# Kernel tuning notes

Measured on AMD Instinct MI355X. Metric: run time of the kernel, lower is better.

## Reference

```python
import jax, jax.numpy as jnp
import numpy as np


def positional_encoding(n_tokens, d_model, dtype=jnp.float32):
    # standard sinusoidal PE: pe[pos, 2i] = sin(pos / 10000^(2i/d)), pe[pos, 2i+1] = cos(...)
    pos = jnp.arange(n_tokens, dtype=dtype)[:, None]            # [n, 1]
    i = jnp.arange(0, d_model, 2, dtype=dtype)[None, :]         # [1, d/2]
    angle = pos / jnp.power(jnp.asarray(10000.0, dtype), i / d_model)
    pe = jnp.zeros((n_tokens, d_model), dtype)
    pe = pe.at[:, 0::2].set(jnp.sin(angle))
    pe = pe.at[:, 1::2].set(jnp.cos(angle))
    return pe


def layer_norm(x, gamma, beta, eps=1e-5):
    mu = jnp.mean(x, axis=-1, keepdims=True)
    var = jnp.var(x, axis=-1, keepdims=True)
    return (x - mu) * jax.lax.rsqrt(var + eps) * gamma + beta


def setup_inputs() -> dict:
    key = jax.random.key(0)
    ks = jax.random.split(key, 4)
    b, n, d = 4, 1024, 1024
    dh = 1024  # dim_hidden_linear
    s = 1.0 / np.sqrt(d)
    return {
        "token_embedding": jax.random.normal(ks[0], (b, n, d), jnp.float32),
        "ln_gamma": jnp.ones((d,), jnp.float32),
        "ln_beta": jnp.zeros((d,), jnp.float32),
        "Wq": jax.random.normal(ks[1], (d, dh), jnp.float32) * s,
        "bq": jnp.zeros((dh,), jnp.float32),
        "Wk": jax.random.normal(ks[2], (d, dh), jnp.float32) * s,
        "bk": jnp.zeros((dh,), jnp.float32),
        "Wv": jax.random.normal(ks[3], (d, dh), jnp.float32) * s,
        "bv": jnp.zeros((dh,), jnp.float32),
        "num_heads": 16,
    }


def reference(token_embedding, ln_gamma, ln_beta, Wq, bq, Wk, bk, Wv, bv, num_heads):
    b, n, d = token_embedding.shape
    pe = positional_encoding(n, d)                      # [n, d]
    x = token_embedding + pe[None, :, :]                # broadcast over batch
    x = layer_norm(x, ln_gamma, ln_beta)
    q = x @ Wq + bq                                     # [b, n, dh]
    k = x @ Wk + bk
    v = x @ Wv + bv
    dh = q.shape[-1]
    hd = dh // num_heads                                # per-head dim
    q = q.reshape(b, n, num_heads, hd)
    k = k.reshape(b, n, num_heads, hd)
    v = v.reshape(b, n, num_heads, hd)
    scale = 1.0 / jnp.sqrt(jnp.asarray(hd, q.dtype))
    scores = jnp.einsum("bqhd,bkhd->bhqk", q, k) * scale  # [b, h, n, n]
    attn = jax.nn.softmax(scores, axis=-1)
    out = jnp.einsum("bhqk,bkhd->bqhd", attn, v)          # [b, n, h, hd]
    return out.reshape(b, n, dh)
```

## Files before the change

kernel.cpp:

```cpp
#include <hip/hip_runtime.h>
#include <hip/hip_bf16.h>
#include <math.h>

typedef __attribute__((ext_vector_type(8))) short bf16x8;
typedef __attribute__((ext_vector_type(4))) short bf16x4;
typedef __attribute__((ext_vector_type(4))) float f32x4;

static __device__ __forceinline__ void gld16(const void* g, void* l) {
    __builtin_amdgcn_global_load_lds(
        (const __attribute__((address_space(1))) unsigned int*)g,
        (__attribute__((address_space(3))) unsigned int*)l, 16, 0, 0);
}

static __device__ __forceinline__ short f2bf_s(float f) {
    __hip_bfloat16 h = __float2bfloat16(f);
    short s;
    __builtin_memcpy(&s, &h, 2);
    return s;
}

__global__ __launch_bounds__(256) void peln_kernel(
    const float* __restrict__ emb,
    const float* __restrict__ gamma,
    const float* __restrict__ beta,
    __hip_bfloat16* __restrict__ x)
{
    const int row = blockIdx.x;
    const int t   = row & 1023;
    const int tid = threadIdx.x;

    float4 e = ((const float4*)(emb + (size_t)row * 1024))[tid];
    float v[4] = {e.x, e.y, e.z, e.w};
    float s = 0.f, ss = 0.f;
    #pragma unroll
    for (int kk = 0; kk < 4; ++kk) {
        int c = tid * 4 + kk;
        float ang = (float)t * exp2f(-13.287712379549449f * (float)(c >> 1) * (1.0f / 512.0f));
        float pe  = (c & 1) ? __cosf(ang) : __sinf(ang);
        v[kk] += pe;
        s  += v[kk];
        ss += v[kk] * v[kk];
    }
    #pragma unroll
    for (int off = 1; off < 64; off <<= 1) {
        s  += __shfl_xor(s, off);
        ss += __shfl_xor(ss, off);
    }
    __shared__ float red_s[4], red_ss[4];
    int wave = tid >> 6, lane = tid & 63;
    if (lane == 0) { red_s[wave] = s; red_ss[wave] = ss; }
    __syncthreads();
    float S  = red_s[0] + red_s[1] + red_s[2] + red_s[3];
    float SS = red_ss[0] + red_ss[1] + red_ss[2] + red_ss[3];
    float mu   = S * (1.0f / 1024.0f);
    float var  = SS * (1.0f / 1024.0f) - mu * mu;
    float rstd = rsqrtf(var + 1e-5f);
    #pragma unroll
    for (int kk = 0; kk < 4; ++kk) {
        int c = tid * 4 + kk;
        float y = (v[kk] - mu) * rstd * gamma[c] + beta[c];
        x[(size_t)row * 1024 + c] = __float2bfloat16(y);
    }
}

__global__ void wt_kernel(const float* __restrict__ Wq,
                          const float* __restrict__ Wk,
                          const float* __restrict__ Wv,
                          __hip_bfloat16* __restrict__ Wt)
{
    __shared__ __hip_bfloat16 tile[32][33];
    int zz = blockIdx.z;
    const float* src = (zz == 0) ? Wq : (zz == 1) ? Wk : Wv;
    __hip_bfloat16* dst = Wt + (size_t)zz * 1024 * 1024;
    int x0 = blockIdx.x * 32, y0 = blockIdx.y * 32;
    int tx = threadIdx.x, ty = threadIdx.y;
    #pragma unroll
    for (int kk = 0; kk < 4; ++kk)
        tile[ty + 8 * kk][tx] =
            __float2bfloat16(src[(size_t)(y0 + ty + 8 * kk) * 1024 + x0 + tx]);
    __syncthreads();
    #pragma unroll
    for (int kk = 0; kk < 4; ++kk)
        dst[(size_t)(x0 + ty + 8 * kk) * 1024 + y0 + tx] = tile[tx][ty + 8 * kk];
}

__global__ __launch_bounds__(256) void qkv_gemm(
    const __hip_bfloat16* __restrict__ X,
    const __hip_bfloat16* __restrict__ Wt,
    const float* __restrict__ bq,
    const float* __restrict__ bk,
    const float* __restrict__ bv,
    __hip_bfloat16* __restrict__ qkv)
{
    union SMem {
        struct { __hip_bfloat16 A[128 * 64]; __hip_bfloat16 B[128 * 64]; } s;
        __hip_bfloat16 C[128 * 132];
    };
    __shared__ __align__(16) SMem sm;

    const int id   = blockIdx.x;
    const int xcd  = id & 7;
    const int rest = id >> 3;
    const int j    = rest % 3;
    const int mblk = rest / 3;
    const int m0   = mblk * 128;
    const int n0   = (xcd * 3 + j) * 128;
    const int t    = n0 >> 10;
    const int nn0  = n0 & 1023;
    const __hip_bfloat16* W = Wt + (size_t)t * 1024 * 1024;

    const int tid  = threadIdx.x;
    const int wave = tid >> 6, lane = tid & 63;
    const int wm = wave & 1, wn = wave >> 1;
    const int lm = lane & 15, quad = lane >> 4;

    const int srow = lane >> 3;
    const int skc  = ((lane & 7) ^ srow) * 8;
    const int rbase = wave * 32;
    const __hip_bfloat16* gA = X + (size_t)(m0 + rbase + srow) * 1024 + skc;
    const __hip_bfloat16* gB = W + (size_t)(nn0 + rbase + srow) * 1024 + skc;
    __hip_bfloat16* lA = sm.s.A + rbase * 64;
    __hip_bfloat16* lB = sm.s.B + rbase * 64;

    f32x4 acc[4][4];
    #pragma unroll
    for (int i = 0; i < 4; ++i)
        #pragma unroll
        for (int jj = 0; jj < 4; ++jj)
            acc[i][jj] = (f32x4){0.f, 0.f, 0.f, 0.f};

    for (int k0 = 0; k0 < 1024; k0 += 64) {
        #pragma unroll
        for (int n = 0; n < 4; ++n) {
            gld16(gA + (size_t)n * 8 * 1024 + k0, lA + n * 8 * 64);
            gld16(gB + (size_t)n * 8 * 1024 + k0, lB + n * 8 * 64);
        }
        __syncthreads();

        bf16x8 a[2][4], b[2][4];
        #pragma unroll
        for (int ks = 0; ks < 2; ++ks) {
            #pragma unroll
            for (int i = 0; i < 4; ++i) {
                int row = wm * 64 + i * 16 + lm;
                a[ks][i] = *(const bf16x8*)(sm.s.A + (size_t)row * 64
                                            + (((ks * 4 + quad) ^ (lm & 7)) * 8));
            }
            #pragma unroll
            for (int jj = 0; jj < 4; ++jj) {
                int row = wn * 64 + jj * 16 + lm;
                b[ks][jj] = *(const bf16x8*)(sm.s.B + (size_t)row * 64
                                             + (((ks * 4 + quad) ^ (lm & 7)) * 8));
            }
        }
        __syncthreads();

        #pragma unroll
        for (int ks = 0; ks < 2; ++ks)
            #pragma unroll
            for (int i = 0; i < 4; ++i)
                #pragma unroll
                for (int jj = 0; jj < 4; ++jj)
                    acc[i][jj] = __builtin_amdgcn_mfma_f32_16x16x32_bf16(a[ks][i], b[ks][jj], acc[i][jj], 0, 0, 0);
    }

    const float* bias = (t == 0) ? bq : (t == 1) ? bk : bv;
    #pragma unroll
    for (int jj = 0; jj < 4; ++jj) {
        int col = wn * 64 + jj * 16 + lm;
        float bb = bias[nn0 + col];
        #pragma unroll
        for (int i = 0; i < 4; ++i)
            #pragma unroll
            for (int r = 0; r < 4; ++r) {
                int row = wm * 64 + i * 16 + quad * 4 + r;
                sm.C[(size_t)row * 132 + col] = __float2bfloat16(acc[i][jj][r] + bb);
            }
    }
    __syncthreads();
    __hip_bfloat16* out = qkv + (size_t)t * 4096 * 1024;
    #pragma unroll
    for (int c = 0; c < 8; ++c) {
        int g = tid + 256 * c;
        int row = g >> 4;
        int colc = (g & 15) * 8;
        bf16x8 vch = *(const bf16x8*)&sm.C[(size_t)row * 132 + colc];
        *(bf16x8*)(out + (size_t)(m0 + row) * 1024 + nn0 + colc) = vch;
    }
}

__global__ void vt_kernel(const __hip_bfloat16* __restrict__ v,
                          __hip_bfloat16* __restrict__ vt)
{
    __shared__ __hip_bfloat16 tile[32][33];
    int bh = blockIdx.z;
    int b = bh >> 4, h = bh & 15;
    int n0 = blockIdx.x * 32, d0 = blockIdx.y * 32;
    int tx = threadIdx.x, ty = threadIdx.y;
    #pragma unroll
    for (int kk = 0; kk < 4; ++kk)
        tile[ty + 8 * kk][tx] =
            v[(size_t)(b * 1024 + n0 + ty + 8 * kk) * 1024 + h * 64 + d0 + tx];
    __syncthreads();
    #pragma unroll
    for (int kk = 0; kk < 4; ++kk)
        vt[((size_t)bh * 64 + d0 + ty + 8 * kk) * 1024 + n0 + tx] = tile[tx][ty + 8 * kk];
}

__global__ __launch_bounds__(256, 2) void attn_kernel(
    const __hip_bfloat16* __restrict__ q,
    const __hip_bfloat16* __restrict__ k,
    const __hip_bfloat16* __restrict__ vt,
    float* __restrict__ out)
{
    __shared__ __align__(16) __hip_bfloat16 Kbuf[64 * 64];
    __shared__ __align__(16) __hip_bfloat16 Vbuf[64 * 64];
    __shared__ short ldsPT[4][32][72];
    const int id   = blockIdx.x;
    const int bh   = (id & 7) * 8 + ((id >> 3) & 7);
    const int qblk = id >> 6;
    const int b = bh >> 4, h = bh & 15;
    const int wave = threadIdx.x >> 6, lane = threadIdx.x & 63;
    const int lm = lane & 15, quad = lane >> 4;
    const int qbase = qblk * 128 + wave * 32;
    const float CEXP = 0.18033688011112042f;

    bf16x8 bqf[2][2];
    #pragma unroll
    for (int i = 0; i < 2; ++i)
        #pragma unroll
        for (int ks = 0; ks < 2; ++ks)
            bqf[i][ks] = *(const bf16x8*)(q + (size_t)(b * 1024 + qbase + 16 * i + lm) * 1024
                                            + h * 64 + ks * 32 + quad * 8);

    const __hip_bfloat16* kg = k + (size_t)(b * 1024) * 1024 + h * 64;
    const __hip_bfloat16* vg = vt + (size_t)bh * 64 * 1024;
    const int srow = lane >> 3;
    const int skc  = ((lane & 7) ^ srow) * 8;

    f32x4 OT[4][2];
    float li[2] = {0.f, 0.f};
    #pragma unroll
    for (int nt = 0; nt < 4; ++nt)
        #pragma unroll
        for (int i = 0; i < 2; ++i)
            OT[nt][i] = (f32x4){0.f, 0.f, 0.f, 0.f};

    for (int kt = 0; kt < 1024; kt += 64) {
        #pragma unroll
        for (int n = 0; n < 2; ++n) {
            int r0 = n * 32 + wave * 8;
            gld16(kg + (size_t)(kt + r0 + srow) * 1024 + skc, Kbuf + r0 * 64);
            gld16(vg + (size_t)(r0 + srow) * 1024 + kt + skc, Vbuf + r0 * 64);
        }
        __syncthreads();

        bf16x8 ak[4][2], av[4][2];
        #pragma unroll
        for (int jt = 0; jt < 4; ++jt)
            #pragma unroll
            for (int ks = 0; ks < 2; ++ks)
                ak[jt][ks] = *(const bf16x8*)(Kbuf + (size_t)(16 * jt + lm) * 64
                                              + (((ks * 4 + quad) ^ (lm & 7)) * 8));
        #pragma unroll
        for (int nt = 0; nt < 4; ++nt)
            #pragma unroll
            for (int ks = 0; ks < 2; ++ks)
                av[nt][ks] = *(const bf16x8*)(Vbuf + (size_t)(16 * nt + lm) * 64
                                              + (((ks * 4 + quad) ^ (lm & 7)) * 8));
        __syncthreads();

        f32x4 ST[2][4];
        #pragma unroll
        for (int i = 0; i < 2; ++i)
            #pragma unroll
            for (int jt = 0; jt < 4; ++jt)
                ST[i][jt] = (f32x4){0.f, 0.f, 0.f, 0.f};
        #pragma unroll
        for (int ks = 0; ks < 2; ++ks)
            #pragma unroll
            for (int i = 0; i < 2; ++i)
                #pragma unroll
                for (int jt = 0; jt < 4; ++jt)
                    ST[i][jt] = __builtin_amdgcn_mfma_f32_16x16x32_bf16(ak[jt][ks], bqf[i][ks], ST[i][jt], 0, 0, 0);

        #pragma unroll
        for (int i = 0; i < 2; ++i)
            #pragma unroll
            for (int jt = 0; jt < 4; ++jt) {
                bf16x4 pk;
                #pragma unroll
                for (int r = 0; r < 4; ++r) {
                    float p = __builtin_amdgcn_exp2f(ST[i][jt][r] * CEXP);
                    li[i] += p;
                    pk[r] = f2bf_s(p);
                }
                *(bf16x4*)&ldsPT[wave][16 * i + lm][16 * jt + quad * 4] = pk;
            }

        bf16x8 bp[2][2];
        #pragma unroll
        for (int i = 0; i < 2; ++i)
            #pragma unroll
            for (int ks = 0; ks < 2; ++ks)
                bp[i][ks] = *(const bf16x8*)&ldsPT[wave][16 * i + lm][ks * 32 + quad * 8];
        #pragma unroll
        for (int ks = 0; ks < 2; ++ks)
            #pragma unroll
            for (int nt = 0; nt < 4; ++nt)
                #pragma unroll
                for (int i = 0; i < 2; ++i)
                    OT[nt][i] = __builtin_amdgcn_mfma_f32_16x16x32_bf16(av[nt][ks], bp[i][ks], OT[nt][i], 0, 0, 0);
    }

    #pragma unroll
    for (int i = 0; i < 2; ++i) {
        li[i] += __shfl_xor(li[i], 16);
        li[i] += __shfl_xor(li[i], 32);
    }

    #pragma unroll
    for (int i = 0; i < 2; ++i) {
        float inv = 1.0f / li[i];
        int qrow = qbase + 16 * i + lm;
        #pragma unroll
        for (int nt = 0; nt < 4; ++nt) {
            float4 o4 = {OT[nt][i][0] * inv, OT[nt][i][1] * inv,
                         OT[nt][i][2] * inv, OT[nt][i][3] * inv};
            *(float4*)(out + (size_t)(b * 1024 + qrow) * 1024 + h * 64 + 16 * nt + quad * 4) = o4;
        }
    }
}

extern "C" void kernel_launch(void* const* d_in, const int* in_sizes, int n_in,
                              void* d_out, int out_size, void* d_ws, size_t ws_size,
                              hipStream_t stream)
{
    const float* emb   = (const float*)d_in[0];
    const float* gamma = (const float*)d_in[1];
    const float* beta  = (const float*)d_in[2];
    const float* Wq    = (const float*)d_in[3];
    const float* bq    = (const float*)d_in[4];
    const float* Wk    = (const float*)d_in[5];
    const float* bk    = (const float*)d_in[6];
    const float* Wv    = (const float*)d_in[7];
    const float* bv    = (const float*)d_in[8];
    float* out = (float*)d_out;

    __hip_bfloat16* ws  = (__hip_bfloat16*)d_ws;
    __hip_bfloat16* x   = ws;
    __hip_bfloat16* Wt  = x   + (size_t)4096 * 1024;
    __hip_bfloat16* qkv = Wt  + (size_t)3 * 1024 * 1024;
    __hip_bfloat16* vt  = qkv + (size_t)3 * 4096 * 1024;

    peln_kernel<<<4096, 256, 0, stream>>>(emb, gamma, beta, x);
    wt_kernel<<<dim3(32, 32, 3), dim3(32, 8), 0, stream>>>(Wq, Wk, Wv, Wt);
    qkv_gemm<<<768, 256, 0, stream>>>(x, Wt, bq, bk, bv, qkv);
    vt_kernel<<<dim3(32, 2, 64), dim3(32, 8), 0, stream>>>(qkv + (size_t)2 * 4096 * 1024, vt);
    attn_kernel<<<512, 256, 0, stream>>>(qkv, qkv + (size_t)4096 * 1024, vt, out);
}
```

Baseline: 165.1 us.

## Fuse weight transpose into LN, write V transposed from GEMM, widen attention K tile

Merges the PE+LayerNorm and weight-transpose kernels into one launch. The QKV GEMM epilogue now writes V directly in transposed per-head layout, which removes the separate V-transpose kernel and its extra pass over memory. The attention loop now stages 128 keys per iteration, halving the number of block-wide barriers at the cost of more LDS per block. Fewer launches and less intermediate traffic are the aim; the transposed LDS store of V may cause bank conflicts.

```diff
diff --git a/kernel.cpp b/kernel.cpp
--- a/kernel.cpp
+++ b/kernel.cpp
@@ -19,69 +19,71 @@
     return s;
 }
 
-__global__ __launch_bounds__(256) void peln_kernel(
+__global__ __launch_bounds__(256) void peln_wt_kernel(
     const float* __restrict__ emb,
     const float* __restrict__ gamma,
     const float* __restrict__ beta,
-    __hip_bfloat16* __restrict__ x)
+    const float* __restrict__ Wq,
+    const float* __restrict__ Wk,
+    const float* __restrict__ Wv,
+    __hip_bfloat16* __restrict__ x,
+    __hip_bfloat16* __restrict__ Wt)
 {
-    const int row = blockIdx.x;
-    const int t   = row & 1023;
     const int tid = threadIdx.x;
-
-    float4 e = ((const float4*)(emb + (size_t)row * 1024))[tid];
-    float v[4] = {e.x, e.y, e.z, e.w};
-    float s = 0.f, ss = 0.f;
-    #pragma unroll
-    for (int kk = 0; kk < 4; ++kk) {
-        int c = tid * 4 + kk;
-        float ang = (float)t * exp2f(-13.287712379549449f * (float)(c >> 1) * (1.0f / 512.0f));
-        float pe  = (c & 1) ? __cosf(ang) : __sinf(ang);
-        v[kk] += pe;
-        s  += v[kk];
-        ss += v[kk] * v[kk];
-    }
-    #pragma unroll
-    for (int off = 1; off < 64; off <<= 1) {
-        s  += __shfl_xor(s, off);
-        ss += __shfl_xor(ss, off);
-    }
-    __shared__ float red_s[4], red_ss[4];
-    int wave = tid >> 6, lane = tid & 63;
-    if (lane == 0) { red_s[wave] = s; red_ss[wave] = ss; }
-    __syncthreads();
-    float S  = red_s[0] + red_s[1] + red_s[2] + red_s[3];
-    float SS = red_ss[0] + red_ss[1] + red_ss[2] + red_ss[3];
-    float mu   = S * (1.0f / 1024.0f);
-    float var  = SS * (1.0f / 1024.0f) - mu * mu;
-    float rstd = rsqrtf(var + 1e-5f);
-    #pragma unroll
-    for (int kk = 0; kk < 4; ++kk) {
-        int c = tid * 4 + kk;
-        float y = (v[kk] - mu) * rstd * gamma[c] + beta[c];
-        x[(size_t)row * 1024 + c] = __float2bfloat16(y);
-    }
-}
-
-__global__ void wt_kernel(const float* __restrict__ Wq,
-                          const float* __restrict__ Wk,
-                          const float* __restrict__ Wv,
-                          __hip_bfloat16* __restrict__ Wt)
-{
-    __shared__ __hip_bfloat16 tile[32][33];
-    int zz = blockIdx.z;
-    const float* src = (zz == 0) ? Wq : (zz == 1) ? Wk : Wv;
-    __hip_bfloat16* dst = Wt + (size_t)zz * 1024 * 1024;
-    int x0 = blockIdx.x * 32, y0 = blockIdx.y * 32;
-    int tx = threadIdx.x, ty = threadIdx.y;
-    #pragma unroll
-    for (int kk = 0; kk < 4; ++kk)
-        tile[ty + 8 * kk][tx] =
-            __float2bfloat16(src[(size_t)(y0 + ty + 8 * kk) * 1024 + x0 + tx]);
-    __syncthreads();
-    #pragma unroll
-    for (int kk = 0; kk < 4; ++kk)
-        dst[(size_t)(x0 + ty + 8 * kk) * 1024 + y0 + tx] = tile[tx][ty + 8 * kk];
+    if (blockIdx.x < 4096) {
+        const int row = blockIdx.x;
+        const int t   = row & 1023;
+        float4 e = ((const float4*)(emb + (size_t)row * 1024))[tid];
+        float v[4] = {e.x, e.y, e.z, e.w};
+        float s = 0.f, ss = 0.f;
+        #pragma unroll
+        for (int kk = 0; kk < 4; ++kk) {
+            int c = tid * 4 + kk;
+            float ang = (float)t * exp2f(-13.287712379549449f * (float)(c >> 1) * (1.0f / 512.0f));
+            float pe  = (c & 1) ? __cosf(ang) : __sinf(ang);
+            v[kk] += pe;
+            s  += v[kk];
+            ss += v[kk] * v[kk];
+        }
+        #pragma unroll
+        for (int off = 1; off < 64; off <<= 1) {
+            s  += __shfl_xor(s, off);
+            ss += __shfl_xor(ss, off);
+        }
+        __shared__ float red_s[4], red_ss[4];
+        int wave = tid >> 6, lane = tid & 63;
+        if (lane == 0) { red_s[wave] = s; red_ss[wave] = ss; }
+        __syncthreads();
+        float S  = red_s[0] + red_s[1] + red_s[2] + red_s[3];
+        float SS = red_ss[0] + red_ss[1] + red_ss[2] + red_ss[3];
+        float mu   = S * (1.0f / 1024.0f);
+        float var  = SS * (1.0f / 1024.0f) - mu * mu;
+        float rstd = rsqrtf(var + 1e-5f);
+        #pragma unroll
+        for (int kk = 0; kk < 4; ++kk) {
+            int c = tid * 4 + kk;
+            float y = (v[kk] - mu) * rstd * gamma[c] + beta[c];
+            x[(size_t)row * 1024 + c] = __float2bfloat16(y);
+        }
+    } else {
+        __shared__ __hip_bfloat16 tile[32][33];
+        int wid = blockIdx.x - 4096;
+        int zz  = wid >> 10;
+        int rem = wid & 1023;
+        int bx = rem & 31, by = rem >> 5;
+        int tx = tid & 31, ty = tid >> 5;
+        const float* src = (zz == 0) ? Wq : (zz == 1) ? Wk : Wv;
+        __hip_bfloat16* dst = Wt + (size_t)zz * 1024 * 1024;
+        int x0 = bx * 32, y0 = by * 32;
+        #pragma unroll
+        for (int kk = 0; kk < 4; ++kk)
+            tile[ty + 8 * kk][tx] =
+                __float2bfloat16(src[(size_t)(y0 + ty + 8 * kk) * 1024 + x0 + tx]);
+        __syncthreads();
+        #pragma unroll
+        for (int kk = 0; kk < 4; ++kk)
+            dst[(size_t)(x0 + ty + 8 * kk) * 1024 + y0 + tx] = tile[tx][ty + 8 * kk];
+    }
 }
 
 __global__ __launch_bounds__(256) void qkv_gemm(
@@ -90,7 +92,8 @@
     const float* __restrict__ bq,
     const float* __restrict__ bk,
     const float* __restrict__ bv,
-    __hip_bfloat16* __restrict__ qkv)
+    __hip_bfloat16* __restrict__ qkv,
+    __hip_bfloat16* __restrict__ vt)
 {
     union SMem {
         struct { __hip_bfloat16 A[128 * 64]; __hip_bfloat16 B[128 * 64]; } s;
@@ -165,46 +168,56 @@
     }
 
     const float* bias = (t == 0) ? bq : (t == 1) ? bk : bv;
-    #pragma unroll
-    for (int jj = 0; jj < 4; ++jj) {
-        int col = wn * 64 + jj * 16 + lm;
-        float bb = bias[nn0 + col];
-        #pragma unroll
-        for (int i = 0; i < 4; ++i)
-            #pragma unroll
-            for (int r = 0; r < 4; ++r) {
-                int row = wm * 64 + i * 16 + quad * 4 + r;
-                sm.C[(size_t)row * 132 + col] = __float2bfloat16(acc[i][jj][r] + bb);
-            }
-    }
-    __syncthreads();
-    __hip_bfloat16* out = qkv + (size_t)t * 4096 * 1024;
-    #pragma unroll
-    for (int c = 0; c < 8; ++c) {
-        int g = tid + 256 * c;
-        int row = g >> 4;
-        int colc = (g & 15) * 8;
-        bf16x8 vch = *(const bf16x8*)&sm.C[(size_t)row * 132 + colc];
-        *(bf16x8*)(out + (size_t)(m0 + row) * 1024 + nn0 + colc) = vch;
-    }
-}
-
-__global__ void vt_kernel(const __hip_bfloat16* __restrict__ v,
-                          __hip_bfloat16* __restrict__ vt)
-{
-    __shared__ __hip_bfloat16 tile[32][33];
-    int bh = blockIdx.z;
-    int b = bh >> 4, h = bh & 15;
-    int n0 = blockIdx.x * 32, d0 = blockIdx.y * 32;
-    int tx = threadIdx.x, ty = threadIdx.y;
-    #pragma unroll
-    for (int kk = 0; kk < 4; ++kk)
-        tile[ty + 8 * kk][tx] =
-            v[(size_t)(b * 1024 + n0 + ty + 8 * kk) * 1024 + h * 64 + d0 + tx];
-    __syncthreads();
-    #pragma unroll
-    for (int kk = 0; kk < 4; ++kk)
-        vt[((size_t)bh * 64 + d0 + ty + 8 * kk) * 1024 + n0 + tx] = tile[tx][ty + 8 * kk];
+    if (t < 2) {
+        #pragma unroll
+        for (int jj = 0; jj < 4; ++jj) {
+            int col = wn * 64 + jj * 16 + lm;
+            float bb = bias[nn0 + col];
+            #pragma unroll
+            for (int i = 0; i < 4; ++i)
+                #pragma unroll
+                for (int r = 0; r < 4; ++r) {
+                    int row = wm * 64 + i * 16 + quad * 4 + r;
+                    sm.C[(size_t)row * 132 + col] = __float2bfloat16(acc[i][jj][r] + bb);
+                }
+        }
+        __syncthreads();
+        __hip_bfloat16* out = qkv + (size_t)t * 4096 * 1024;
+        #pragma unroll
+        for (int c = 0; c < 8; ++c) {
+            int g = tid + 256 * c;
+            int row = g >> 4;
+            int colc = (g & 15) * 8;
+            bf16x8 vch = *(const bf16x8*)&sm.C[(size_t)row * 132 + colc];
+            *(bf16x8*)(out + (size_t)(m0 + row) * 1024 + nn0 + colc) = vch;
+        }
+    } else {
+        #pragma unroll
+        for (int jj = 0; jj < 4; ++jj) {
+            int col = wn * 64 + jj * 16 + lm;
+            float bb = bias[nn0 + col];
+            #pragma unroll
+            for (int i = 0; i < 4; ++i)
+                #pragma unroll
+                for (int r = 0; r < 4; ++r) {
+                    int row = wm * 64 + i * 16 + quad * 4 + r;
+                    sm.C[(size_t)col * 132 + row] = __float2bfloat16(acc[i][jj][r] + bb);
+                }
+        }
+        __syncthreads();
+        const int bbase = (m0 >> 10) * 16 + (nn0 >> 6);
+        const int mloc  = m0 & 1023;
+        #pragma unroll
+        for (int c = 0; c < 8; ++c) {
+            int g = tid + 256 * c;
+            int col = g >> 4;
+            int rch = (g & 15) * 8;
+            bf16x8 vch = *(const bf16x8*)&sm.C[(size_t)col * 132 + rch];
+            int bh = bbase + (col >> 6);
+            int d  = col & 63;
+            *(bf16x8*)(vt + ((size_t)bh * 64 + d) * 1024 + mloc + rch) = vch;
+        }
+    }
 }
 
 __global__ __launch_bounds__(256, 2) void attn_kernel(
@@ -213,8 +226,8 @@
     const __hip_bfloat16* __restrict__ vt,
     float* __restrict__ out)
 {
-    __shared__ __align__(16) __hip_bfloat16 Kbuf[64 * 64];
-    __shared__ __align__(16) __hip_bfloat16 Vbuf[64 * 64];
+    __shared__ __align__(16) __hip_bfloat16 Kbuf[128 * 64];
+    __shared__ __align__(16) __hip_bfloat16 Vbuf[2][64 * 64];
     __shared__ short ldsPT[4][32][72];
     const int id   = blockIdx.x;
     const int bh   = (id & 7) * 8 + ((id >> 3) & 7);
@@ -246,71 +259,82 @@
         for (int i = 0; i < 2; ++i)
             OT[nt][i] = (f32x4){0.f, 0.f, 0.f, 0.f};
 
-    for (int kt = 0; kt < 1024; kt += 64) {
-        #pragma unroll
-        for (int n = 0; n < 2; ++n) {
-            int r0 = n * 32 + wave * 8;
+    for (int kt = 0; kt < 1024; kt += 128) {
+        #pragma unroll
+        for (int n = 0; n < 4; ++n) {
+            int r0 = wave * 32 + n * 8;
             gld16(kg + (size_t)(kt + r0 + srow) * 1024 + skc, Kbuf + r0 * 64);
-            gld16(vg + (size_t)(r0 + srow) * 1024 + kt + skc, Vbuf + r0 * 64);
-        }
-        __syncthreads();
-
-        bf16x8 ak[4][2], av[4][2];
-        #pragma unroll
-        for (int jt = 0; jt < 4; ++jt)
+        }
+        {
+            int half = wave >> 1;
+            #pragma unroll
+            for (int n = 0; n < 4; ++n) {
+                int d0 = (wave & 1) * 32 + n * 8;
+                gld16(vg + (size_t)(d0 + srow) * 1024 + kt + half * 64 + skc,
+                      Vbuf[half] + d0 * 64);
+            }
+        }
+        __syncthreads();
+
+        #pragma unroll
+        for (int sr = 0; sr < 2; ++sr) {
+            bf16x8 ak[4][2], av[4][2];
+            #pragma unroll
+            for (int jt = 0; jt < 4; ++jt)
+                #pragma unroll
+                for (int ks = 0; ks < 2; ++ks)
+                    ak[jt][ks] = *(const bf16x8*)(Kbuf + (size_t)(sr * 64 + 16 * jt + lm) * 64
+                                                  + (((ks * 4 + quad) ^ (lm & 7)) * 8));
+            #pragma unroll
+            for (int nt = 0; nt < 4; ++nt)
+                #pragma unroll
+                for (int ks = 0; ks < 2; ++ks)
+                    av[nt][ks] = *(const bf16x8*)(Vbuf[sr] + (size_t)(16 * nt + lm) * 64
+                                                  + (((ks * 4 + quad) ^ (lm & 7)) * 8));
+            if (sr == 1) __syncthreads();
+
+            f32x4 ST[2][4];
+            #pragma unroll
+            for (int i = 0; i < 2; ++i)
+                #pragma unroll
+                for (int jt = 0; jt < 4; ++jt)
+                    ST[i][jt] = (f32x4){0.f, 0.f, 0.f, 0.f};
             #pragma unroll
             for (int ks = 0; ks < 2; ++ks)
-                ak[jt][ks] = *(const bf16x8*)(Kbuf + (size_t)(16 * jt + lm) * 64
-                                              + (((ks * 4 + quad) ^ (lm & 7)) * 8));
-        #pragma unroll
-        for (int nt = 0; nt < 4; ++nt)
+                #pragma unroll
+                for (int i = 0; i < 2; ++i)
+                    #pragma unroll
+                    for (int jt = 0; jt < 4; ++jt)
+                        ST[i][jt] = __builtin_amdgcn_mfma_f32_16x16x32_bf16(ak[jt][ks], bqf[i][ks], ST[i][jt], 0, 0, 0);
+
+            #pragma unroll
+            for (int i = 0; i < 2; ++i)
+                #pragma unroll
+                for (int jt = 0; jt < 4; ++jt) {
+                    bf16x4 pk;
+                    #pragma unroll
+                    for (int r = 0; r < 4; ++r) {
+                        float p = __builtin_amdgcn_exp2f(ST[i][jt][r] * CEXP);
+                        li[i] += p;
+                        pk[r] = f2bf_s(p);
+                    }
+                    *(bf16x4*)&ldsPT[wave][16 * i + lm][16 * jt + quad * 4] = pk;
+                }
+
+            bf16x8 bp[2][2];
+            #pragma unroll
+            for (int i = 0; i < 2; ++i)
+                #pragma unroll
+                for (int ks = 0; ks < 2; ++ks)
+                    bp[i][ks] = *(const bf16x8*)&ldsPT[wave][16 * i + lm][ks * 32 + quad * 8];
             #pragma unroll
             for (int ks = 0; ks < 2; ++ks)
-                av[nt][ks] = *(const bf16x8*)(Vbuf + (size_t)(16 * nt + lm) * 64
-                                              + (((ks * 4 + quad) ^ (lm & 7)) * 8));
-        __syncthreads();
-
-        f32x4 ST[2][4];
-        #pragma unroll
-        for (int i = 0; i < 2; ++i)
-            #pragma unroll
-            for (int jt = 0; jt < 4; ++jt)
-                ST[i][jt] = (f32x4){0.f, 0.f, 0.f, 0.f};
-        #pragma unroll
-        for (int ks = 0; ks < 2; ++ks)
-            #pragma unroll
-            for (int i = 0; i < 2; ++i)
-                #pragma unroll
-                for (int jt = 0; jt < 4; ++jt)
-                    ST[i][jt] = __builtin_amdgcn_mfma_f32_16x16x32_bf16(ak[jt][ks], bqf[i][ks], ST[i][jt], 0, 0, 0);
-
-        #pragma unroll
-        for (int i = 0; i < 2; ++i)
-            #pragma unroll
-            for (int jt = 0; jt < 4; ++jt) {
-                bf16x4 pk;
-                #pragma unroll
-                for (int r = 0; r < 4; ++r) {
-                    float p = __builtin_amdgcn_exp2f(ST[i][jt][r] * CEXP);
-                    li[i] += p;
-                    pk[r] = f2bf_s(p);
-                }
-                *(bf16x4*)&ldsPT[wave][16 * i + lm][16 * jt + quad * 4] = pk;
-            }
-
-        bf16x8 bp[2][2];
-        #pragma unroll
-        for (int i = 0; i < 2; ++i)
-            #pragma unroll
-            for (int ks = 0; ks < 2; ++ks)
-                bp[i][ks] = *(const bf16x8*)&ldsPT[wave][16 * i + lm][ks * 32 + quad * 8];
-        #pragma unroll
-        for (int ks = 0; ks < 2; ++ks)
-            #pragma unroll
-            for (int nt = 0; nt < 4; ++nt)
-                #pragma unroll
-                for (int i = 0; i < 2; ++i)
-                    OT[nt][i] = __builtin_amdgcn_mfma_f32_16x16x32_bf16(av[nt][ks], bp[i][ks], OT[nt][i], 0, 0, 0);
+                #pragma unroll
+                for (int nt = 0; nt < 4; ++nt)
+                    #pragma unroll
+                    for (int i = 0; i < 2; ++i)
+                        OT[nt][i] = __builtin_amdgcn_mfma_f32_16x16x32_bf16(av[nt][ks], bp[i][ks], OT[nt][i], 0, 0, 0);
+        }
     }
 
     #pragma unroll
@@ -351,11 +375,9 @@
     __hip_bfloat16* x   = ws;
     __hip_bfloat16* Wt  = x   + (size_t)4096 * 1024;
     __hip_bfloat16* qkv = Wt  + (size_t)3 * 1024 * 1024;
-    __hip_bfloat16* vt  = qkv + (size_t)3 * 4096 * 1024;
-
-    peln_kernel<<<4096, 256, 0, stream>>>(emb, gamma, beta, x);
-    wt_kernel<<<dim3(32, 32, 3), dim3(32, 8), 0, stream>>>(Wq, Wk, Wv, Wt);
-    qkv_gemm<<<768, 256, 0, stream>>>(x, Wt, bq, bk, bv, qkv);
-    vt_kernel<<<dim3(32, 2, 64), dim3(32, 8), 0, stream>>>(qkv + (size_t)2 * 4096 * 1024, vt);
+    __hip_bfloat16* vt  = qkv + (size_t)2 * 4096 * 1024;
+
+    peln_wt_kernel<<<4096 + 3072, 256, 0, stream>>>(emb, gamma, beta, Wq, Wk, Wv, x, Wt);
+    qkv_gemm<<<768, 256, 0, stream>>>(x, Wt, bq, bk, bv, qkv, vt);
     attn_kernel<<<512, 256, 0, stream>>>(qkv, qkv + (size_t)4096 * 1024, vt, out);
 }
```

Measured after the change: 156.0 us. 1.06x faster.
